# Kernel tuning notes

Measured on AMD Instinct MI355X. Metric: run time of the kernel, lower is better.

## Reference

```python
import jax, jax.numpy as jnp
import numpy as np

SOFT_BLEND = 20.0
INIT_BONES = np.array([0, 1, 2, 4, 5, 16, 17, 18, 19])
MAX_STEPS = 20
CVG_THRESH = 1e-5
DVG_THRESH = 1.0
EPS = 1e-6


def mlp(x, W0, b0, W1, b1, W2, b2):
    h = jax.nn.softplus(x @ W0 + b0)
    h = jax.nn.softplus(h @ W1 + b1)
    return h @ W2 + b2


def query_weights(x, params):
    # lbs_network -> soft_blend * logits -> softmax  (softmax_mode='softmax')
    return jax.nn.softmax(SOFT_BLEND * mlp(x, *params), axis=-1)


def forward_skinning(xc, params, tfs):
    # xc [B,N,3], tfs [B,J,4,4] -> xd [B,N,3]  (LBS: blend transforms with weights)
    w = query_weights(xc, params)                                    # [B,N,J]
    xh = jnp.concatenate([xc, jnp.ones_like(xc[..., :1])], -1)       # [B,N,4]
    return jnp.einsum('bpn,bnij,bpj->bpi', w, tfs, xh)[..., :3]


def gradient(xc, params, tfs):
    # per-point jacobian d(forward_skinning)/d(xc): [B,N,3,3]
    def f(x, tfs_b):
        w = query_weights(x, params)                                 # [J]
        xh = jnp.concatenate([x, jnp.ones((1,), x.dtype)])
        return jnp.einsum('j,jik,k->i', w, tfs_b, xh)[:3]
    jac = jax.jacfwd(f)
    return jax.vmap(jax.vmap(jac, in_axes=(0, None)), in_axes=(0, 0))(xc, tfs)


def broyden(g, x_init, J_inv_init):
    # vectorized Broyden: the torch data-dependent boolean masking becomes
    # mask-gated jnp.where updates; the early break becomes a fixed-length scan
    # (iterations are no-ops once ids_val is all False).
    x = x_init                                                       # [M,3,1]
    J_inv = J_inv_init                                               # [M,3,3]
    gx = g(x)
    update = -(J_inv @ gx)
    gx_norm_opt = jnp.linalg.norm(gx[..., 0], axis=-1)               # [M]
    state = (x, gx, J_inv, update, gx_norm_opt,
             jnp.zeros_like(x), jnp.zeros_like(gx),
             jnp.ones_like(gx_norm_opt, dtype=bool))

    def step(s, _):
        x, gx, J_inv, update, gx_norm_opt, delta_x, delta_gx, ids_val = s
        m = ids_val[:, None, None]
        delta_x = jnp.where(m, update, delta_x)
        x = x + jnp.where(m, delta_x, 0.0)
        gx_new = g(x)
        delta_gx = jnp.where(m, gx_new - gx, delta_gx)
        gx = jnp.where(m, gx_new, gx)
        gx_norm = jnp.linalg.norm(gx[..., 0], axis=-1)
        ids_opt = gx_norm < gx_norm_opt
        gx_norm_opt = jnp.where(ids_opt, gx_norm, gx_norm_opt)
        ids_val = (gx_norm_opt > CVG_THRESH) & (gx_norm < DVG_THRESH)
        m2 = ids_val[:, None, None]
        vT = jnp.swapaxes(delta_x, -1, -2) @ J_inv                   # [M,1,3]
        a = delta_x - J_inv @ delta_gx                               # [M,3,1]
        b = vT @ delta_gx                                            # [M,1,1]
        b = b + jnp.where(b >= 0, EPS, -EPS)
        J_inv = J_inv + jnp.where(m2, (a / b) @ vT, 0.0)
        update = -(J_inv @ gx)
        return (x, gx, J_inv, update, gx_norm_opt, delta_x, delta_gx, ids_val), None

    state, _ = jax.lax.scan(step, state, None, length=MAX_STEPS)
    # in the torch code x_opt aliases x, so the returned root is the final x
    return state[0], state[4]


def _forward(xd, tfs, W0, b0, W1, b1, W2, b2):
    params = (W0, b0, W1, b1, W2, b2)
    sg = jax.lax.stop_gradient
    B, N, D = xd.shape
    I = len(INIT_BONES)
    # ---- init: inverse rigid transform per init bone (one-hot weights) ----
    xdh = jnp.concatenate([xd, jnp.ones_like(xd[..., :1])], -1)      # [B,N,4]
    T_inv = jnp.linalg.inv(tfs[:, INIT_BONES])                        # [B,I,4,4]
    xc_init = jnp.einsum('bcij,bnj->bnci', T_inv, xdh)[..., :3]       # [B,N,I,3]
    # ---- Broyden correspondence search (torch.no_grad) ----
    params_sg = tuple(sg(p) for p in params)
    tfs_sg = sg(tfs)
    xc_flat = sg(xc_init).reshape(B, N * I, D)
    xd_tgt = sg(jnp.repeat(xd, I, axis=1))                            # [B,N*I,3]
    J_inv_init = jnp.linalg.inv(gradient(xc_flat, params_sg, tfs_sg)).reshape(-1, D, D)

    def g(x):                                                         # [M,3,1] -> [M,3,1]
        xc = x[..., 0].reshape(B, N * I, D)
        err = forward_skinning(xc, params_sg, tfs_sg) - xd_tgt
        return err.reshape(-1, D, 1)

    x_opt, _ = broyden(g, xc_flat.reshape(-1, D, 1), J_inv_init)
    xc_opt = sg(x_opt[..., 0].reshape(B, N * I, D))
    # ---- implicit differentiation correction term ----
    xd_opt = forward_skinning(xc_opt, params, tfs)
    grad_inv = sg(jnp.linalg.inv(gradient(xc_opt, params, tfs)))      # [B,M,3,3]
    correction = xd_opt - sg(xd_opt)
    correction = jnp.einsum('bnij,bnj->bni', -grad_inv, correction)
    return (xc_opt + correction).reshape(B, N, I, D)


def setup_inputs():
    key = jax.random.key(0)
    ks = jax.random.split(key, 6)
    B, N, J, W = 1, 30000, 24, 64
    xd = 0.5 * jax.random.normal(ks[0], (B, N, 3), jnp.float32)
    # near-rigid bone transforms: identity + small perturbation, homogeneous last row
    R = jnp.eye(3, dtype=jnp.float32) + 0.1 * jax.random.normal(ks[1], (B, J, 3, 3), jnp.float32)
    t = 0.2 * jax.random.normal(ks[2], (B, J, 3, 1), jnp.float32)
    bot = jnp.broadcast_to(jnp.array([0., 0., 0., 1.], jnp.float32), (B, J, 1, 4))
    tfs = jnp.concatenate([jnp.concatenate([R, t], -1), bot], -2)     # [B,J,4,4]
    W0 = 0.5 * jax.random.normal(ks[3], (3, W), jnp.float32)
    W1 = jax.random.normal(ks[4], (W, W), jnp.float32) / float(np.sqrt(W))
    W2 = 0.1 * jax.random.normal(ks[5], (W, J), jnp.float32) / float(np.sqrt(W))
    return {"xd": xd, "tfs": tfs,
            "W0": W0, "b0": jnp.zeros((W,), jnp.float32),
            "W1": W1, "b1": jnp.zeros((W,), jnp.float32),
            "W2": W2, "b2": jnp.zeros((J,), jnp.float32)}


def reference(xd, tfs, W0, b0, W1, b1, W2, b2):
    return _forward(xd, tfs, W0, b0, W1, b1, W2, b2)
```

## Files before the change

### kernel.cpp

```cpp
#include <hip/hip_runtime.h>
#include <math.h>

#define TPB 64
#define NPT 270000
#define SOFTB 20.0f
#define CVGT 1e-5f
#define DVGT 1.0f
#define EPSB 1e-6f

#define WS_TINV 0
#define WS_W0T  256

__global__ void prep_kernel(const float* __restrict__ tfs,
                            const float* __restrict__ W0, const float* __restrict__ b0,
                            float* __restrict__ ws) {
    int t = threadIdx.x;
    if (t < 9) {
        const int bones[9] = {0, 1, 2, 4, 5, 16, 17, 18, 19};
        const float* T = tfs + bones[t] * 16;
        float r00=T[0], r01=T[1], r02=T[2],  t0=T[3];
        float r10=T[4], r11=T[5], r12=T[6],  t1=T[7];
        float r20=T[8], r21=T[9], r22=T[10], t2=T[11];
        float c00 = r11*r22 - r12*r21;
        float c01 = r12*r20 - r10*r22;
        float c02 = r10*r21 - r11*r20;
        float det = r00*c00 + r01*c01 + r02*c02;
        float id  = 1.0f / det;
        float i00=c00*id, i01=(r02*r21-r01*r22)*id, i02=(r01*r12-r02*r11)*id;
        float i10=c01*id, i11=(r00*r22-r02*r20)*id, i12=(r02*r10-r00*r12)*id;
        float i20=c02*id, i21=(r01*r20-r00*r21)*id, i22=(r00*r11-r01*r10)*id;
        float* O = ws + WS_TINV + t * 16;
        O[0]=i00; O[1]=i01; O[2]=i02;  O[3]=-(i00*t0+i01*t1+i02*t2);
        O[4]=i10; O[5]=i11; O[6]=i12;  O[7]=-(i10*t0+i11*t1+i12*t2);
        O[8]=i20; O[9]=i21; O[10]=i22; O[11]=-(i20*t0+i21*t1+i22*t2);
        O[12]=0.f; O[13]=0.f; O[14]=0.f; O[15]=1.f;
    }
    for (int i = t; i < 64*4; i += 256) {
        int k = i >> 2, cidx = i & 3;
        ws[WS_W0T + i] = (cidx < 3) ? W0[cidx*64 + k] : b0[k];
    }
}

__global__ __launch_bounds__(TPB)
__attribute__((amdgpu_waves_per_eu(4, 4)))
void deform_kernel(
    const float* __restrict__ xd,
    const float* __restrict__ tfs,
    const float* __restrict__ W1, const float* __restrict__ b1,
    const float* __restrict__ W2, const float* __restrict__ b2,
    const float* __restrict__ ws,
    float* __restrict__ out)
{
    __shared__ float lds[33 * TPB];
    const int tid = threadIdx.x;
    const int p   = blockIdx.x * TPB + tid;
    const bool live = (p < NPT);
    const int pc = live ? p : 0;
    const int n  = pc / 9;
    const int c  = pc - n * 9;

    const float tx0 = xd[n*3+0], tx1 = xd[n*3+1], tx2 = xd[n*3+2];

    const float* Ti  = ws + WS_TINV + c * 16;
    const float* W0T = ws + WS_W0T;

    float x0 = fmaf(Ti[0], tx0, fmaf(Ti[1], tx1, fmaf(Ti[2],  tx2, Ti[3])));
    float x1 = fmaf(Ti[4], tx0, fmaf(Ti[5], tx1, fmaf(Ti[6],  tx2, Ti[7])));
    float x2 = fmaf(Ti[8], tx0, fmaf(Ti[9], tx1, fmaf(Ti[10], tx2, Ti[11])));

    float h1[64];

    auto forward = [&](float a0, float a1, float a2, float& o0, float& o1, float& o2) {
        #pragma unroll
        for (int j = 0; j < 64; ++j) h1[j] = b1[j];
        #pragma unroll 2
        for (int k = 0; k < 64; ++k) {
            float w0a = W0T[k*4+0], w0b = W0T[k*4+1], w0c = W0T[k*4+2], w0d = W0T[k*4+3];
            float z  = fmaf(a0, w0a, fmaf(a1, w0b, fmaf(a2, w0c, w0d)));
            float hk = fmaxf(z, 0.f) + __logf(1.f + __expf(-fabsf(z)));
            const float* Wr = W1 + k*64;
            #pragma unroll
            for (int j = 0; j < 64; ++j) h1[j] = fmaf(hk, Wr[j], h1[j]);
        }
        #pragma unroll
        for (int j = 0; j < 64; ++j) {
            float z = h1[j];
            h1[j] = fmaxf(z, 0.f) + __logf(1.f + __expf(-fabsf(z)));
        }
        float mo[24];
        #pragma unroll
        for (int q = 0; q < 24; ++q) mo[q] = b2[q];
        #pragma unroll 2
        for (int k = 0; k < 64; ++k) {
            float hk = h1[k];
            const float* Wr = W2 + k*24;
            #pragma unroll
            for (int q = 0; q < 24; ++q) mo[q] = fmaf(hk, Wr[q], mo[q]);
        }
        float mx = mo[0];
        #pragma unroll
        for (int q = 1; q < 24; ++q) mx = fmaxf(mx, mo[q]);
        float ssum = 0.f;
        #pragma unroll
        for (int q = 0; q < 24; ++q) { float e = __expf(SOFTB*(mo[q]-mx)); mo[q] = e; ssum += e; }
        float inv = 1.0f / ssum;
        o0 = 0.f; o1 = 0.f; o2 = 0.f;
        #pragma unroll
        for (int q = 0; q < 24; ++q) {
            float wq = mo[q] * inv;
            lds[q*TPB + tid] = wq;
            const float* Tn = tfs + q*16;
            float y0 = fmaf(Tn[0], a0, fmaf(Tn[1], a1, fmaf(Tn[2],  a2, Tn[3])));
            float y1 = fmaf(Tn[4], a0, fmaf(Tn[5], a1, fmaf(Tn[6],  a2, Tn[7])));
            float y2 = fmaf(Tn[8], a0, fmaf(Tn[9], a1, fmaf(Tn[10], a2, Tn[11])));
            o0 = fmaf(wq, y0, o0); o1 = fmaf(wq, y1, o1); o2 = fmaf(wq, y2, o2);
        }
    };

    float f0, f1, f2;
    forward(x0, x1, x2, f0, f1, f2);

    #pragma unroll
    for (int j = 0; j < 64; ++j) h1[j] = 1.0f - __expf(-h1[j]);

    for (int t = 0; t < 3; ++t) {
        float dm[24];
        #pragma unroll
        for (int q = 0; q < 24; ++q) dm[q] = 0.f;
        #pragma unroll
        for (int cc = 0; cc < 4; ++cc) {
            float d1c[16];
            #pragma unroll
            for (int j = 0; j < 16; ++j) d1c[j] = 0.f;
            #pragma unroll 2
            for (int k = 0; k < 64; ++k) {
                float w0a = W0T[k*4+0], w0b = W0T[k*4+1], w0c = W0T[k*4+2], w0d = W0T[k*4+3];
                float z  = fmaf(x0, w0a, fmaf(x1, w0b, fmaf(x2, w0c, w0d)));
                float sg = 1.0f / (1.0f + __expf(-z));
                float dh0 = sg * W0T[k*4 + t];
                const float* Wr = W1 + k*64 + cc*16;
                #pragma unroll
                for (int j = 0; j < 16; ++j) d1c[j] = fmaf(dh0, Wr[j], d1c[j]);
            }
            #pragma unroll
            for (int j = 0; j < 16; ++j) {
                float dh1 = d1c[j] * h1[cc*16 + j];
                const float* Wr = W2 + (cc*16 + j)*24;
                #pragma unroll
                for (int q = 0; q < 24; ++q) dm[q] = fmaf(dh1, Wr[q], dm[q]);
            }
        }
        float dot=0.f, sA=0.f, sB=0.f, sC=0.f, ab0=0.f, ab1=0.f, ab2=0.f;
        #pragma unroll
        for (int q = 0; q < 24; ++q) {
            float wq = lds[q*TPB + tid];
            float wd = wq * dm[q];
            dot += wd;
            const float* Tn = tfs + q*16;
            float y0 = fmaf(Tn[0], x0, fmaf(Tn[1], x1, fmaf(Tn[2],  x2, Tn[3])));
            float y1 = fmaf(Tn[4], x0, fmaf(Tn[5], x1, fmaf(Tn[6],  x2, Tn[7])));
            float y2 = fmaf(Tn[8], x0, fmaf(Tn[9], x1, fmaf(Tn[10], x2, Tn[11])));
            sA = fmaf(wd, y0, sA); sB = fmaf(wd, y1, sB); sC = fmaf(wd, y2, sC);
            ab0 = fmaf(wq, Tn[0 + t], ab0);
            ab1 = fmaf(wq, Tn[4 + t], ab1);
            ab2 = fmaf(wq, Tn[8 + t], ab2);
        }
        lds[(24 + 0*3 + t)*TPB + tid] = ab0 + SOFTB*(sA - dot*f0);
        lds[(24 + 1*3 + t)*TPB + tid] = ab1 + SOFTB*(sB - dot*f1);
        lds[(24 + 2*3 + t)*TPB + tid] = ab2 + SOFTB*(sC - dot*f2);
    }

    float m00 = lds[(24+0)*TPB+tid], m01 = lds[(24+1)*TPB+tid], m02 = lds[(24+2)*TPB+tid];
    float m10 = lds[(24+3)*TPB+tid], m11 = lds[(24+4)*TPB+tid], m12 = lds[(24+5)*TPB+tid];
    float m20 = lds[(24+6)*TPB+tid], m21 = lds[(24+7)*TPB+tid], m22 = lds[(24+8)*TPB+tid];
    float c00 = m11*m22 - m12*m21, c01 = m12*m20 - m10*m22, c02 = m10*m21 - m11*m20;
    float det = m00*c00 + m01*c01 + m02*c02;
    float idet = 1.0f / det;
    float Ji0=c00*idet, Ji1=(m02*m21-m01*m22)*idet, Ji2=(m01*m12-m02*m11)*idet;
    float Ji3=c01*idet, Ji4=(m00*m22-m02*m20)*idet, Ji5=(m02*m10-m00*m12)*idet;
    float Ji6=c02*idet, Ji7=(m01*m20-m00*m21)*idet, Ji8=(m00*m11-m01*m10)*idet;

    float g0 = f0 - tx0, g1 = f1 - tx1, g2 = f2 - tx2;
    float gno = sqrtf(g0*g0 + g1*g1 + g2*g2);
    float u0 = -(Ji0*g0 + Ji1*g1 + Ji2*g2);
    float u1 = -(Ji3*g0 + Ji4*g1 + Ji5*g2);
    float u2 = -(Ji6*g0 + Ji7*g1 + Ji8*g2);
    bool valid = true;

    for (int it = 0; it < 20; ++it) {
        if (!__any((int)valid)) break;
        if (valid) {
            float dx0 = u0, dx1 = u1, dx2 = u2;
            x0 += dx0; x1 += dx1; x2 += dx2;
            float fn0, fn1, fn2;
            forward(x0, x1, x2, fn0, fn1, fn2);
            float ng0 = fn0 - tx0, ng1 = fn1 - tx1, ng2 = fn2 - tx2;
            float dg0 = ng0 - g0, dg1 = ng1 - g1, dg2 = ng2 - g2;
            g0 = ng0; g1 = ng1; g2 = ng2;
            float gn = sqrtf(g0*g0 + g1*g1 + g2*g2);
            gno = fminf(gn, gno);
            valid = (gno > CVGT) && (gn < DVGT);
            if (valid) {
                float v0 = dx0*Ji0 + dx1*Ji3 + dx2*Ji6;
                float v1 = dx0*Ji1 + dx1*Ji4 + dx2*Ji7;
                float v2 = dx0*Ji2 + dx1*Ji5 + dx2*Ji8;
                float a0 = dx0 - (Ji0*dg0 + Ji1*dg1 + Ji2*dg2);
                float a1 = dx1 - (Ji3*dg0 + Ji4*dg1 + Ji5*dg2);
                float a2 = dx2 - (Ji6*dg0 + Ji7*dg1 + Ji8*dg2);
                float b = v0*dg0 + v1*dg1 + v2*dg2;
                b += (b >= 0.f) ? EPSB : -EPSB;
                float ib = 1.0f / b;
                a0 *= ib; a1 *= ib; a2 *= ib;
                Ji0 = fmaf(a0, v0, Ji0); Ji1 = fmaf(a0, v1, Ji1); Ji2 = fmaf(a0, v2, Ji2);
                Ji3 = fmaf(a1, v0, Ji3); Ji4 = fmaf(a1, v1, Ji4); Ji5 = fmaf(a1, v2, Ji5);
                Ji6 = fmaf(a2, v0, Ji6); Ji7 = fmaf(a2, v1, Ji7); Ji8 = fmaf(a2, v2, Ji8);
                u0 = -(Ji0*g0 + Ji1*g1 + Ji2*g2);
                u1 = -(Ji3*g0 + Ji4*g1 + Ji5*g2);
                u2 = -(Ji6*g0 + Ji7*g1 + Ji8*g2);
            }
        }
    }

    if (live) {
        out[p*3+0] = x0;
        out[p*3+1] = x1;
        out[p*3+2] = x2;
    }
}

extern "C" void kernel_launch(void* const* d_in, const int* in_sizes, int n_in,
                              void* d_out, int out_size, void* d_ws, size_t ws_size,
                              hipStream_t stream) {
    const float* xd  = (const float*)d_in[0];
    const float* tfs = (const float*)d_in[1];
    const float* W0  = (const float*)d_in[2];
    const float* b0  = (const float*)d_in[3];
    const float* W1  = (const float*)d_in[4];
    const float* b1  = (const float*)d_in[5];
    const float* W2  = (const float*)d_in[6];
    const float* b2  = (const float*)d_in[7];
    float* out = (float*)d_out;
    float* ws  = (float*)d_ws;

    prep_kernel<<<1, 256, 0, stream>>>(tfs, W0, b0, ws);
    int nblk = (NPT + TPB - 1) / TPB;
    deform_kernel<<<nblk, TPB, 0, stream>>>(xd, tfs, W1, b1, W2, b2, ws, out);
}
```

Measured before the change: 872.7 us.

## Recompute layer-1 activations in Jacobian loop to drop h1 registers and LDS

The 64-entry hidden-activation array is no longer kept live across the Jacobian computation. Layer-1 pre-activations are now recomputed in 16-wide chunks inside each of the three derivative passes, and the forward pass is fused chunkwise into the layer-2 accumulation. Softmax weights and Jacobian entries stay in registers instead of LDS, and the fixed waves-per-EU attribute is removed. The aim is lower register pressure and higher occupancy, at the cost of roughly doubling the layer-1 FMA work and repeating the transform evaluations in each derivative pass.

```diff
diff --git a/kernel.cpp b/kernel.cpp
--- a/kernel.cpp
+++ b/kernel.cpp
@@ -41,9 +41,7 @@
     }
 }
 
-__global__ __launch_bounds__(TPB)
-__attribute__((amdgpu_waves_per_eu(4, 4)))
-void deform_kernel(
+__global__ __launch_bounds__(TPB) void deform_kernel(
     const float* __restrict__ xd,
     const float* __restrict__ tfs,
     const float* __restrict__ W1, const float* __restrict__ b1,
@@ -51,7 +49,6 @@
     const float* __restrict__ ws,
     float* __restrict__ out)
 {
-    __shared__ float lds[33 * TPB];
     const int tid = threadIdx.x;
     const int p   = blockIdx.x * TPB + tid;
     const bool live = (p < NPT);
@@ -68,47 +65,47 @@
     float x1 = fmaf(Ti[4], tx0, fmaf(Ti[5], tx1, fmaf(Ti[6],  tx2, Ti[7])));
     float x2 = fmaf(Ti[8], tx0, fmaf(Ti[9], tx1, fmaf(Ti[10], tx2, Ti[11])));
 
-    float h1[64];
+    float wreg[24];
 
     auto forward = [&](float a0, float a1, float a2, float& o0, float& o1, float& o2) {
         #pragma unroll
-        for (int j = 0; j < 64; ++j) h1[j] = b1[j];
-        #pragma unroll 2
-        for (int k = 0; k < 64; ++k) {
-            float w0a = W0T[k*4+0], w0b = W0T[k*4+1], w0c = W0T[k*4+2], w0d = W0T[k*4+3];
-            float z  = fmaf(a0, w0a, fmaf(a1, w0b, fmaf(a2, w0c, w0d)));
-            float hk = fmaxf(z, 0.f) + __logf(1.f + __expf(-fabsf(z)));
-            const float* Wr = W1 + k*64;
-            #pragma unroll
-            for (int j = 0; j < 64; ++j) h1[j] = fmaf(hk, Wr[j], h1[j]);
-        }
-        #pragma unroll
-        for (int j = 0; j < 64; ++j) {
-            float z = h1[j];
-            h1[j] = fmaxf(z, 0.f) + __logf(1.f + __expf(-fabsf(z)));
-        }
-        float mo[24];
-        #pragma unroll
-        for (int q = 0; q < 24; ++q) mo[q] = b2[q];
-        #pragma unroll 2
-        for (int k = 0; k < 64; ++k) {
-            float hk = h1[k];
-            const float* Wr = W2 + k*24;
-            #pragma unroll
-            for (int q = 0; q < 24; ++q) mo[q] = fmaf(hk, Wr[q], mo[q]);
-        }
-        float mx = mo[0];
-        #pragma unroll
-        for (int q = 1; q < 24; ++q) mx = fmaxf(mx, mo[q]);
+        for (int q = 0; q < 24; ++q) wreg[q] = b2[q];
+        #pragma unroll 1
+        for (int cc = 0; cc < 4; ++cc) {
+            float z1c[16];
+            const float* b1c = b1 + cc*16;
+            #pragma unroll
+            for (int j = 0; j < 16; ++j) z1c[j] = b1c[j];
+            #pragma unroll 2
+            for (int k = 0; k < 64; ++k) {
+                float w0a = W0T[k*4+0], w0b = W0T[k*4+1], w0c = W0T[k*4+2], w0d = W0T[k*4+3];
+                float z  = fmaf(a0, w0a, fmaf(a1, w0b, fmaf(a2, w0c, w0d)));
+                float hk = fmaxf(z, 0.f) + __logf(1.f + __expf(-fabsf(z)));
+                const float* Wr = W1 + k*64 + cc*16;
+                #pragma unroll
+                for (int j = 0; j < 16; ++j) z1c[j] = fmaf(hk, Wr[j], z1c[j]);
+            }
+            #pragma unroll
+            for (int j = 0; j < 16; ++j) {
+                float zz = z1c[j];
+                float h  = fmaxf(zz, 0.f) + __logf(1.f + __expf(-fabsf(zz)));
+                const float* W2r = W2 + (cc*16 + j)*24;
+                #pragma unroll
+                for (int q = 0; q < 24; ++q) wreg[q] = fmaf(h, W2r[q], wreg[q]);
+            }
+        }
+        float mx = wreg[0];
+        #pragma unroll
+        for (int q = 1; q < 24; ++q) mx = fmaxf(mx, wreg[q]);
         float ssum = 0.f;
         #pragma unroll
-        for (int q = 0; q < 24; ++q) { float e = __expf(SOFTB*(mo[q]-mx)); mo[q] = e; ssum += e; }
+        for (int q = 0; q < 24; ++q) { float e = __expf(SOFTB*(wreg[q]-mx)); wreg[q] = e; ssum += e; }
         float inv = 1.0f / ssum;
         o0 = 0.f; o1 = 0.f; o2 = 0.f;
         #pragma unroll
         for (int q = 0; q < 24; ++q) {
-            float wq = mo[q] * inv;
-            lds[q*TPB + tid] = wq;
+            float wq = wreg[q] * inv;
+            wreg[q] = wq;
             const float* Tn = tfs + q*16;
             float y0 = fmaf(Tn[0], a0, fmaf(Tn[1], a1, fmaf(Tn[2],  a2, Tn[3])));
             float y1 = fmaf(Tn[4], a0, fmaf(Tn[5], a1, fmaf(Tn[6],  a2, Tn[7])));
@@ -120,59 +117,71 @@
     float f0, f1, f2;
     forward(x0, x1, x2, f0, f1, f2);
 
-    #pragma unroll
-    for (int j = 0; j < 64; ++j) h1[j] = 1.0f - __expf(-h1[j]);
-
+    float Jm[9];
+    #pragma unroll 1
     for (int t = 0; t < 3; ++t) {
-        float dm[24];
-        #pragma unroll
-        for (int q = 0; q < 24; ++q) dm[q] = 0.f;
-        #pragma unroll
+        float dot = 0.f, sA = 0.f, sB = 0.f, sC = 0.f;
+        #pragma unroll 1
         for (int cc = 0; cc < 4; ++cc) {
-            float d1c[16];
-            #pragma unroll
-            for (int j = 0; j < 16; ++j) d1c[j] = 0.f;
+            float z1c[16], d1c[16];
+            const float* b1c = b1 + cc*16;
+            #pragma unroll
+            for (int j = 0; j < 16; ++j) { z1c[j] = b1c[j]; d1c[j] = 0.f; }
             #pragma unroll 2
             for (int k = 0; k < 64; ++k) {
                 float w0a = W0T[k*4+0], w0b = W0T[k*4+1], w0c = W0T[k*4+2], w0d = W0T[k*4+3];
+                float wt  = W0T[k*4 + t];
                 float z  = fmaf(x0, w0a, fmaf(x1, w0b, fmaf(x2, w0c, w0d)));
-                float sg = 1.0f / (1.0f + __expf(-z));
-                float dh0 = sg * W0T[k*4 + t];
+                float e  = __expf(-z);
+                float hk = z + __logf(1.f + e);
+                float sg = 1.0f / (1.0f + e);
+                float dh0 = sg * wt;
                 const float* Wr = W1 + k*64 + cc*16;
                 #pragma unroll
-                for (int j = 0; j < 16; ++j) d1c[j] = fmaf(dh0, Wr[j], d1c[j]);
-            }
+                for (int j = 0; j < 16; ++j) {
+                    z1c[j] = fmaf(hk,  Wr[j], z1c[j]);
+                    d1c[j] = fmaf(dh0, Wr[j], d1c[j]);
+                }
+            }
+            float dmc[24];
+            #pragma unroll
+            for (int q = 0; q < 24; ++q) dmc[q] = 0.f;
             #pragma unroll
             for (int j = 0; j < 16; ++j) {
-                float dh1 = d1c[j] * h1[cc*16 + j];
-                const float* Wr = W2 + (cc*16 + j)*24;
-                #pragma unroll
-                for (int q = 0; q < 24; ++q) dm[q] = fmaf(dh1, Wr[q], dm[q]);
-            }
-        }
-        float dot=0.f, sA=0.f, sB=0.f, sC=0.f, ab0=0.f, ab1=0.f, ab2=0.f;
+                float sg1 = 1.0f / (1.0f + __expf(-z1c[j]));
+                float dh1 = d1c[j] * sg1;
+                const float* W2r = W2 + (cc*16 + j)*24;
+                #pragma unroll
+                for (int q = 0; q < 24; ++q) dmc[q] = fmaf(dh1, W2r[q], dmc[q]);
+            }
+            #pragma unroll
+            for (int q = 0; q < 24; ++q) {
+                float wd = wreg[q] * dmc[q];
+                dot += wd;
+                const float* Tn = tfs + q*16;
+                float y0 = fmaf(Tn[0], x0, fmaf(Tn[1], x1, fmaf(Tn[2],  x2, Tn[3])));
+                float y1 = fmaf(Tn[4], x0, fmaf(Tn[5], x1, fmaf(Tn[6],  x2, Tn[7])));
+                float y2 = fmaf(Tn[8], x0, fmaf(Tn[9], x1, fmaf(Tn[10], x2, Tn[11])));
+                sA = fmaf(wd, y0, sA); sB = fmaf(wd, y1, sB); sC = fmaf(wd, y2, sC);
+            }
+        }
+        float ab0 = 0.f, ab1 = 0.f, ab2 = 0.f;
         #pragma unroll
         for (int q = 0; q < 24; ++q) {
-            float wq = lds[q*TPB + tid];
-            float wd = wq * dm[q];
-            dot += wd;
+            float wq = wreg[q];
             const float* Tn = tfs + q*16;
-            float y0 = fmaf(Tn[0], x0, fmaf(Tn[1], x1, fmaf(Tn[2],  x2, Tn[3])));
-            float y1 = fmaf(Tn[4], x0, fmaf(Tn[5], x1, fmaf(Tn[6],  x2, Tn[7])));
-            float y2 = fmaf(Tn[8], x0, fmaf(Tn[9], x1, fmaf(Tn[10], x2, Tn[11])));
-            sA = fmaf(wd, y0, sA); sB = fmaf(wd, y1, sB); sC = fmaf(wd, y2, sC);
             ab0 = fmaf(wq, Tn[0 + t], ab0);
             ab1 = fmaf(wq, Tn[4 + t], ab1);
             ab2 = fmaf(wq, Tn[8 + t], ab2);
         }
-        lds[(24 + 0*3 + t)*TPB + tid] = ab0 + SOFTB*(sA - dot*f0);
-        lds[(24 + 1*3 + t)*TPB + tid] = ab1 + SOFTB*(sB - dot*f1);
-        lds[(24 + 2*3 + t)*TPB + tid] = ab2 + SOFTB*(sC - dot*f2);
-    }
-
-    float m00 = lds[(24+0)*TPB+tid], m01 = lds[(24+1)*TPB+tid], m02 = lds[(24+2)*TPB+tid];
-    float m10 = lds[(24+3)*TPB+tid], m11 = lds[(24+4)*TPB+tid], m12 = lds[(24+5)*TPB+tid];
-    float m20 = lds[(24+6)*TPB+tid], m21 = lds[(24+7)*TPB+tid], m22 = lds[(24+8)*TPB+tid];
+        Jm[0 + t] = ab0 + SOFTB*(sA - dot*f0);
+        Jm[3 + t] = ab1 + SOFTB*(sB - dot*f1);
+        Jm[6 + t] = ab2 + SOFTB*(sC - dot*f2);
+    }
+
+    float m00=Jm[0], m01=Jm[1], m02=Jm[2];
+    float m10=Jm[3], m11=Jm[4], m12=Jm[5];
+    float m20=Jm[6], m21=Jm[7], m22=Jm[8];
     float c00 = m11*m22 - m12*m21, c01 = m12*m20 - m10*m22, c02 = m10*m21 - m11*m20;
     float det = m00*c00 + m01*c01 + m02*c02;
     float idet = 1.0f / det;
```

Result: slower. 947.4 us (+8.6%).
